# Kernel tuning notes

Measured on AMD Instinct MI355X. Metric: run time of the kernel, lower is better.

## Reference

```python
import jax, jax.numpy as jnp
import numpy as np

N, Z, CC = 32, 128, 16
NODE_SIZES = [128, 512, 2048, 8192, 32768, 67615]  # coarse -> fine
IN_CHS = [144, 80, 48, 32, 24]   # FGL input channels (after content concat)
OUT_CHS = [64, 32, 16, 8, 1]     # FGL output channels
N_S, N_T, N_C = 20, 50, 200
EPS = 1e-5


def setup_inputs() -> dict:
    key = jax.random.key(0)
    ks = jax.random.split(key, 64)
    d = {}
    d['z'] = jax.random.normal(ks[0], (N, Z), jnp.float32)
    d['svec'] = jax.random.randint(ks[1], (N,), 0, N_S)
    d['tvec'] = jax.random.randint(ks[2], (N,), 0, N_T)
    d['cvec'] = jax.random.randint(ks[3], (N,), 0, N_C)
    d['study_emb'] = 0.1 * jax.random.normal(ks[4], (N_S, CC), jnp.float32)
    d['task_emb'] = 0.1 * jax.random.normal(ks[5], (N_T, CC), jnp.float32)
    d['contrast_emb'] = 0.1 * jax.random.normal(ks[6], (N_C, CC), jnp.float32)
    fc_ins = [CC, 2 * CC, 3 * CC, 3 * CC, 3 * CC]
    for i, fi in enumerate(fc_ins):
        d[f'fc{i}_w'] = jax.random.normal(ks[7 + i], (fi, CC), jnp.float32) / np.sqrt(fi)
        d[f'fc{i}_b'] = jnp.zeros((CC,), jnp.float32)
    for i in range(5):
        d[f'w{i}'] = jax.random.normal(ks[12 + i], (OUT_CHS[i], IN_CHS[i]), jnp.float32) / np.sqrt(IN_CHS[i])
        d[f'bb{i}'] = jnp.zeros((OUT_CHS[i],), jnp.float32)
    for i in range(4):
        d[f'g{i}'] = jnp.ones((OUT_CHS[i],), jnp.float32)
        d[f'be{i}'] = jnp.zeros((OUT_CHS[i],), jnp.float32)
    # tree upsampling: each fine node has exactly one coarse parent
    for i in range(5):
        d[f'p{i}'] = jax.random.randint(ks[20 + i], (NODE_SIZES[i + 1],), 0, NODE_SIZES[i])
    return d


def _forward(z, svec, tvec, cvec, study_emb, task_emb, contrast_emb,
             fc0_w, fc0_b, fc1_w, fc1_b, fc2_w, fc2_b, fc3_w, fc3_b, fc4_w, fc4_b,
             w0, bb0, w1, bb1, w2, bb2, w3, bb3, w4, bb4,
             g0, be0, g1, be1, g2, be2, g3, be3,
             p0, p1, p2, p3, p4):
    se = study_emb[svec]
    te = task_emb[tvec]
    ce = contrast_emb[cvec]
    cat2 = jnp.concatenate([se, te], axis=1)
    cat3 = jnp.concatenate([se, te, ce], axis=1)
    contents = [se @ fc0_w + fc0_b,
                cat2 @ fc1_w + fc1_b,
                cat3 @ fc2_w + fc2_b,
                cat3 @ fc3_w + fc3_b,
                cat3 @ fc4_w + fc4_b]  # each (N, CC); dropout is identity at eval
    n = z.shape[0]
    cur = jnp.broadcast_to(z[:, :, None], (n, Z, NODE_SIZES[0]))  # (N, 128, 128)
    Ws = [w0, w1, w2, w3, w4]
    bs = [bb0, bb1, bb2, bb3, bb4]
    parents = [p0, p1, p2, p3, p4]
    bns = [(g0, be0), (g1, be1), (g2, be2), (g3, be3)]
    for i in range(5):
        c = jnp.broadcast_to(contents[i][:, :, None], (n, CC, cur.shape[2]))
        x = jnp.concatenate([cur, c], axis=1)  # (N, IN_CHS[i], nodes_in)
        # shared per-layer channel mix; mix first (cheaper), then gather by parent
        h = jnp.einsum('ncj,oc->noj', x, Ws[i]) + bs[i][None, :, None]
        cur = h[:, :, parents[i]]  # (N, OUT_CHS[i], nodes_out)
        if i < 4:
            cur = jnp.where(cur >= 0, cur, 0.2 * cur)  # LeakyReLU(0.2)
            g, be = bns[i]
            mean = cur.mean(axis=(0, 2), keepdims=True)
            var = cur.var(axis=(0, 2), keepdims=True)
            cur = g[None, :, None] * (cur - mean) * jax.lax.rsqrt(var + EPS) + be[None, :, None]
        else:
            cur = jnp.tanh(cur)
    return cur[:, 0, :]  # (N, masked_nnz)


def reference(z, svec, tvec, cvec, study_emb, task_emb, contrast_emb,
              fc0_w, fc0_b, fc1_w, fc1_b, fc2_w, fc2_b, fc3_w, fc3_b, fc4_w, fc4_b,
              w0, bb0, w1, bb1, w2, bb2, w3, bb3, w4, bb4,
              g0, be0, g1, be1, g2, be2, g3, be3,
              p0, p1, p2, p3, p4):
    return _forward(z, svec, tvec, cvec, study_emb, task_emb, contrast_emb,
                    fc0_w, fc0_b, fc1_w, fc1_b, fc2_w, fc2_b, fc3_w, fc3_b, fc4_w, fc4_b,
                    w0, bb0, w1, bb1, w2, bb2, w3, bb3, w4, bb4,
                    g0, be0, g1, be1, g2, be2, g3, be3,
                    p0, p1, p2, p3, p4)
```

## Files before the change

### kernel.cpp

```cpp
#include <hip/hip_runtime.h>
#include <hip/hip_bf16.h>

typedef __hip_bfloat16 bf16;
#define NT 512
#define ROW 67615


__device__ __forceinline__ float lo16(unsigned int u) {
  return __builtin_bit_cast(float, u << 16);
}
__device__ __forceinline__ float hi16(unsigned int u) {
  return __builtin_bit_cast(float, u & 0xFFFF0000u);
}
__device__ __forceinline__ float bs2f(unsigned short u) {
  return __builtin_bit_cast(float, ((unsigned int)u) << 16);
}
__device__ __forceinline__ unsigned short f2bs(float f) {
  return __builtin_bit_cast(unsigned short, __float2bfloat16(f));
}
__device__ __forceinline__ float gld(const void* p, int i, int isbf) {
  if (isbf) return bs2f(((const unsigned short*)p)[i]);
  return ((const float*)p)[i];
}

__device__ __forceinline__ void stage_us(unsigned short* dst, const void* src,
                                         int len, int isbf, int tid) {
  if (isbf) {
    const unsigned short* s = (const unsigned short*)src;
    for (int i = tid; i < len; i += NT) dst[i] = s[i];
  } else {
    const float* s = (const float*)src;
    for (int i = tid; i < len; i += NT) dst[i] = f2bs(s[i]);
  }
}

__device__ __forceinline__ void stageW_rt(unsigned short* dst, const void* src,
                                          int OUT, int COLS, int isbf, int tid) {
  int oshift = 31 - __clz(OUT);
  int tasks = OUT * (COLS >> 2);
  for (int j = tid; j < tasks; j += NT) {
    int o = j & (OUT - 1), c4 = j >> oshift;
    ushort4 q;
    if (isbf) {
      q = *(const ushort4*)((const unsigned short*)src + o * COLS + 4 * c4);
    } else {
      float4 v = *(const float4*)((const float*)src + o * COLS + 4 * c4);
      q = make_ushort4(f2bs(v.x), f2bs(v.y), f2bs(v.z), f2bs(v.w));
    }
    *(ushort4*)(dst + (c4 * OUT + o) * 4) = q;
  }
}

struct Params {
  const void* z;
  const int *sv, *tv, *cv;
  const void *se, *te, *ce;
  const void *fcw[5], *fcb[5];
  const void *w[5],  *wb[5];
  const void *g[4],  *be[4];
  float* t;
};

__device__ __noinline__ void do_level(
    int tid, int isbf, int INC, int OUT, int FCIN, int IS,
    const float* __restrict__ curin, float* __restrict__ curout,
    float* __restrict__ cont, const float* __restrict__ cat,
    float* __restrict__ A, float* __restrict__ Bv,
    unsigned short* __restrict__ wl,
    const void* fcw, const void* fcb, const void* W, const void* Wb,
    const void* g, const void* be, float* __restrict__ tout)
{
  const int OFF_FCB = FCIN * 16;
  const int OFF_W   = OFF_FCB + 16;
  const int OFF_WB  = OFF_W + (INC + 16) * OUT;

  stage_us(wl, fcw, FCIN * 16, isbf, tid);
  stage_us(wl + OFF_FCB, fcb, 16, isbf, tid);
  if (OUT == 1) {
    stage_us(wl + OFF_W, W, INC + 16, isbf, tid);
    stage_us(wl + OFF_WB, Wb, 1, isbf, tid);
  } else {
    stageW_rt(wl + OFF_W, W, OUT, INC + 16, isbf, tid);
    stage_us(wl + OFF_WB, Wb, OUT, isbf, tid);
    stage_us(wl + OFF_WB + OUT, g, OUT, isbf, tid);
    stage_us(wl + OFF_WB + 2 * OUT, be, OUT, isbf, tid);
  }
  __syncthreads();

  if (tid < 128) {
    int n = tid >> 2, cg = tid & 3;
    float a0 = bs2f(wl[OFF_FCB + 4 * cg]);
    float a1 = bs2f(wl[OFF_FCB + 4 * cg + 1]);
    float a2 = bs2f(wl[OFF_FCB + 4 * cg + 2]);
    float a3 = bs2f(wl[OFF_FCB + 4 * cg + 3]);
    const float4* catp = (const float4*)(cat + n * 52);
    int nk4 = FCIN >> 2;
#pragma unroll 4
    for (int k4 = 0; k4 < nk4; k4++) {
      float4 cv = catp[k4];
      float xs[4] = {cv.x, cv.y, cv.z, cv.w};
#pragma unroll
      for (int j = 0; j < 4; j++) {
        uint2 u = *(const uint2*)(wl + (4 * k4 + j) * 16 + 4 * cg);
        a0 += xs[j] * lo16(u.x); a1 += xs[j] * hi16(u.x);
        a2 += xs[j] * lo16(u.y); a3 += xs[j] * hi16(u.y);
      }
    }
    *(float4*)(cont + n * 20 + 4 * cg) = make_float4(a0, a1, a2, a3);
  }
  __syncthreads();

  if (OUT == 1) {
    if (tid < 32) {
      int n = tid;
      float s = bs2f(wl[OFF_WB]);
#pragma unroll
      for (int c = 0; c < 8; c++) s += curin[n * 68 + c] * bs2f(wl[OFF_W + c]);
#pragma unroll
      for (int k = 0; k < 16; k++) s += cont[n * 20 + k] * bs2f(wl[OFF_W + 8 + k]);
      tout[n] = tanhf(s);
    }
    return;
  }

  int TO = OUT >> 1;
  int toshift = 31 - __clz(TO);
  const uint4* Wp = (const uint4*)(wl + OFF_W);
  if (tid < 16 * TO) {
    int tn = tid >> toshift, to = tid & (TO - 1);
    int n0 = 2 * tn, o0 = 2 * to;
    const float4* X0 = (const float4*)(curin + n0 * IS);
    const float4* X1 = (const float4*)(curin + (n0 + 1) * IS);
    const float4* C0 = (const float4*)(cont + n0 * 20);
    const float4* C1 = (const float4*)(cont + (n0 + 1) * 20);
    float b0 = bs2f(wl[OFF_WB + o0]), b1 = bs2f(wl[OFF_WB + o0 + 1]);
    float s00 = b0, s01 = b1, s10 = b0, s11 = b1;
    int nc4 = INC >> 2;
#pragma unroll 4
    for (int c4 = 0; c4 < nc4; c4++) {
      float4 xa = X0[c4], xb = X1[c4];
      uint4 u = Wp[c4 * TO + to];
      float wa0 = lo16(u.x), wa1 = hi16(u.x), wa2 = lo16(u.y), wa3 = hi16(u.y);
      float wb0 = lo16(u.z), wb1 = hi16(u.z), wb2 = lo16(u.w), wb3 = hi16(u.w);
      s00 += xa.x * wa0 + xa.y * wa1 + xa.z * wa2 + xa.w * wa3;
      s01 += xa.x * wb0 + xa.y * wb1 + xa.z * wb2 + xa.w * wb3;
      s10 += xb.x * wa0 + xb.y * wa1 + xb.z * wa2 + xb.w * wa3;
      s11 += xb.x * wb0 + xb.y * wb1 + xb.z * wb2 + xb.w * wb3;
    }
#pragma unroll 4
    for (int k4 = 0; k4 < 4; k4++) {
      float4 xa = C0[k4], xb = C1[k4];
      uint4 u = Wp[(nc4 + k4) * TO + to];
      float wa0 = lo16(u.x), wa1 = hi16(u.x), wa2 = lo16(u.y), wa3 = hi16(u.y);
      float wb0 = lo16(u.z), wb1 = hi16(u.z), wb2 = lo16(u.w), wb3 = hi16(u.w);
      s00 += xa.x * wa0 + xa.y * wa1 + xa.z * wa2 + xa.w * wa3;
      s01 += xa.x * wb0 + xa.y * wb1 + xa.z * wb2 + xa.w * wb3;
      s10 += xb.x * wa0 + xb.y * wa1 + xb.z * wa2 + xb.w * wa3;
      s11 += xb.x * wb0 + xb.y * wb1 + xb.z * wb2 + xb.w * wb3;
    }
    s00 = s00 >= 0.f ? s00 : 0.2f * s00;
    s01 = s01 >= 0.f ? s01 : 0.2f * s01;
    s10 = s10 >= 0.f ? s10 : 0.2f * s10;
    s11 = s11 >= 0.f ? s11 : 0.2f * s11;
    curout[n0 * 68 + o0]           = s00;
    curout[n0 * 68 + o0 + 1]       = s01;
    curout[(n0 + 1) * 68 + o0]     = s10;
    curout[(n0 + 1) * 68 + o0 + 1] = s11;
  }
  __syncthreads();

  if (tid < OUT) {
    int o = tid;
    float su = 0.f, sq = 0.f;
#pragma unroll 4
    for (int n = 0; n < 32; n++) { float v = curout[n * 68 + o]; su += v; sq += v * v; }
    float mean = su * (1.f / 32.f);
    float var  = fmaxf(sq * (1.f / 32.f) - mean * mean, 0.f);
    float inv  = rsqrtf(var + 1e-5f);
    float a = bs2f(wl[OFF_WB + OUT + o]) * inv;
    A[o]  = a;
    Bv[o] = bs2f(wl[OFF_WB + 2 * OUT + o]) - mean * a;
  }
  __syncthreads();
  for (int i = tid; i < 32 * OUT; i += NT) {
    int n = i >> (toshift + 1), o = i & (OUT - 1);
    curout[n * 68 + o] = A[o] * curout[n * 68 + o] + Bv[o];
  }
  __syncthreads();
}

__global__ __launch_bounds__(NT) void head_kernel(Params P) {
  __shared__ __align__(16) float zl[32 * 128];
  __shared__ __align__(16) float cat[32 * 52];
  __shared__ __align__(16) float cont[32 * 20];
  __shared__ __align__(16) float act0[32 * 68];
  __shared__ __align__(16) float act1[32 * 68];
  __shared__ float A[64], Bv[64];
  __shared__ __align__(16) unsigned short wl[9680];
  __shared__ int sOK;
  int tid = threadIdx.x;

  if (tid == 0) sOK = 1;
  __syncthreads();
  if (tid < 64) {
    unsigned int w = ((const unsigned int*)P.z)[tid];
    float a = fabsf(bs2f((unsigned short)(w & 0xFFFFu)));
    if (!(a == 0.0f || (a >= 1e-12f && a <= 1e4f))) atomicAnd(&sOK, 0);
  }
  __syncthreads();
  const int isbf = sOK;
  if (tid == 0) ((int*)P.t)[32] = isbf;

  if (isbf) {
    const uint4* s = (const uint4*)P.z;
    for (int j = tid; j < 512; j += NT) {
      uint4 u = s[j];
      *(float4*)(zl + 8 * j)     = make_float4(lo16(u.x), hi16(u.x), lo16(u.y), hi16(u.y));
      *(float4*)(zl + 8 * j + 4) = make_float4(lo16(u.z), hi16(u.z), lo16(u.w), hi16(u.w));
    }
  } else {
    const float4* s = (const float4*)P.z;
    for (int j = tid; j < 1024; j += NT) *(float4*)(zl + 4 * j) = s[j];
  }
  if (tid < 512) {
    int n = tid >> 4, c = tid & 15;
    cat[n * 52 + c]      = gld(P.se, P.sv[n] * 16 + c, isbf);
    cat[n * 52 + 16 + c] = gld(P.te, P.tv[n] * 16 + c, isbf);
    cat[n * 52 + 32 + c] = gld(P.ce, P.cv[n] * 16 + c, isbf);
  }

  do_level(tid, isbf, 128, 64, 16, 128, zl,   act0, cont, cat, A, Bv, wl,
           P.fcw[0], P.fcb[0], P.w[0], P.wb[0], P.g[0], P.be[0], P.t);
  do_level(tid, isbf,  64, 32, 32,  68, act0, act1, cont, cat, A, Bv, wl,
           P.fcw[1], P.fcb[1], P.w[1], P.wb[1], P.g[1], P.be[1], P.t);
  do_level(tid, isbf,  32, 16, 48,  68, act1, act0, cont, cat, A, Bv, wl,
           P.fcw[2], P.fcb[2], P.w[2], P.wb[2], P.g[2], P.be[2], P.t);
  do_level(tid, isbf,  16,  8, 48,  68, act0, act1, cont, cat, A, Bv, wl,
           P.fcw[3], P.fcb[3], P.w[3], P.wb[3], P.g[3], P.be[3], P.t);
  do_level(tid, isbf,   8,  1, 48,  68, act1, act0, cont, cat, A, Bv, wl,
           P.fcw[4], P.fcb[4], P.w[4], P.wb[4], P.g[0], P.be[0], P.t);
}

__global__ __launch_bounds__(256) void bcast_kernel(const float* __restrict__ t,
                                                    void* __restrict__ outv) {
  int n = blockIdx.y;
  int isbf = ((const int*)t)[32];
  float tv = t[n];
  int chunk = blockIdx.x * 256 + threadIdx.x;

  if (isbf) {
    unsigned short us = f2bs(tv);
    unsigned int u2 = ((unsigned int)us << 16) | (unsigned int)us;
    uint4 v4 = make_uint4(u2, u2, u2, u2);
    unsigned short* row = (unsigned short*)outv + (size_t)n * ROW;
    int s = (int)((16u - ((unsigned int)(unsigned long long)row & 15u)) & 15u) >> 1;
    int e = s + chunk * 8;
    if (e + 8 <= ROW) *(uint4*)(row + e) = v4;
    if (blockIdx.x == 0 && threadIdx.x == 0) {
      for (int i = 0; i < s; i++) row[i] = us;
      int nch = (ROW - s) >> 3;
      for (int i = s + nch * 8; i < ROW; i++) row[i] = us;
    }
  } else {
    float* row = (float*)outv + (size_t)n * ROW;
    int s = (int)((16u - ((unsigned int)(unsigned long long)row & 15u)) & 15u) >> 2;
    int e = s + chunk * 4;
    if (e + 4 <= ROW) *(float4*)(row + e) = make_float4(tv, tv, tv, tv);
    if (blockIdx.x == 0 && threadIdx.x == 0) {
      for (int i = 0; i < s; i++) row[i] = tv;
      int nch = (ROW - s) >> 2;
      for (int i = s + nch * 4; i < ROW; i++) row[i] = tv;
    }
  }
}

extern "C" void kernel_launch(void* const* d_in, const int* in_sizes, int n_in,
                              void* d_out, int out_size, void* d_ws, size_t ws_size,
                              hipStream_t stream) {
  Params P;
  P.z  = d_in[0];
  P.sv = (const int*)d_in[1];
  P.tv = (const int*)d_in[2];
  P.cv = (const int*)d_in[3];
  P.se = d_in[4];
  P.te = d_in[5];
  P.ce = d_in[6];
  for (int i = 0; i < 5; i++) {
    P.fcw[i] = d_in[7 + 2 * i];
    P.fcb[i] = d_in[8 + 2 * i];
  }
  for (int i = 0; i < 5; i++) {
    P.w[i]  = d_in[17 + 2 * i];
    P.wb[i] = d_in[18 + 2 * i];
  }
  for (int i = 0; i < 4; i++) {
    P.g[i]  = d_in[27 + 2 * i];
    P.be[i] = d_in[28 + 2 * i];
  }
  P.t = (float*)d_ws;

  hipLaunchKernelGGL(head_kernel, dim3(1), dim3(NT), 0, stream, P);
  hipLaunchKernelGGL(bcast_kernel, dim3(67, 32), dim3(256), 0, stream,
                     (const float*)d_ws, d_out);
}
```

Baseline: 168.3 us.

## Fuse head MLP and broadcast into one kernel with redundant per-block head

Merges the single-block head kernel and the broadcast kernel into one launch. Each of the 8x32 blocks recomputes the small MLP/BN chain redundantly, then writes its chunk of one output row. All levels' weights are staged into shared memory in one pass, and all five content FCs are computed together. Levels are templated for compile-time sizes and full unrolling. This removes a kernel launch and the workspace round trip, at the cost of repeating the head work in every block and using more dynamic shared memory.

```diff
diff --git a/kernel.cpp b/kernel.cpp
--- a/kernel.cpp
+++ b/kernel.cpp
@@ -58,86 +58,37 @@
   const void *fcw[5], *fcb[5];
   const void *w[5],  *wb[5];
   const void *g[4],  *be[4];
-  float* t;
+  void* out;
 };
 
-__device__ __noinline__ void do_level(
-    int tid, int isbf, int INC, int OUT, int FCIN, int IS,
+#define WLB0 0
+#define WLB1 9680
+#define WLB2 12864
+#define WLB3 14464
+#define WLB4 15528
+#define WL_TOT 16344
+
+template<int INC, int OUT, int IS>
+__device__ __forceinline__ void level_bn(int tid,
     const float* __restrict__ curin, float* __restrict__ curout,
-    float* __restrict__ cont, const float* __restrict__ cat,
-    float* __restrict__ A, float* __restrict__ Bv,
-    unsigned short* __restrict__ wl,
-    const void* fcw, const void* fcb, const void* W, const void* Wb,
-    const void* g, const void* be, float* __restrict__ tout)
+    const float* __restrict__ contl, const unsigned short* __restrict__ wlv,
+    float* __restrict__ A, float* __restrict__ Bv)
 {
-  const int OFF_FCB = FCIN * 16;
-  const int OFF_W   = OFF_FCB + 16;
-  const int OFF_WB  = OFF_W + (INC + 16) * OUT;
-
-  stage_us(wl, fcw, FCIN * 16, isbf, tid);
-  stage_us(wl + OFF_FCB, fcb, 16, isbf, tid);
-  if (OUT == 1) {
-    stage_us(wl + OFF_W, W, INC + 16, isbf, tid);
-    stage_us(wl + OFF_WB, Wb, 1, isbf, tid);
-  } else {
-    stageW_rt(wl + OFF_W, W, OUT, INC + 16, isbf, tid);
-    stage_us(wl + OFF_WB, Wb, OUT, isbf, tid);
-    stage_us(wl + OFF_WB + OUT, g, OUT, isbf, tid);
-    stage_us(wl + OFF_WB + 2 * OUT, be, OUT, isbf, tid);
-  }
-  __syncthreads();
-
-  if (tid < 128) {
-    int n = tid >> 2, cg = tid & 3;
-    float a0 = bs2f(wl[OFF_FCB + 4 * cg]);
-    float a1 = bs2f(wl[OFF_FCB + 4 * cg + 1]);
-    float a2 = bs2f(wl[OFF_FCB + 4 * cg + 2]);
-    float a3 = bs2f(wl[OFF_FCB + 4 * cg + 3]);
-    const float4* catp = (const float4*)(cat + n * 52);
-    int nk4 = FCIN >> 2;
-#pragma unroll 4
-    for (int k4 = 0; k4 < nk4; k4++) {
-      float4 cv = catp[k4];
-      float xs[4] = {cv.x, cv.y, cv.z, cv.w};
-#pragma unroll
-      for (int j = 0; j < 4; j++) {
-        uint2 u = *(const uint2*)(wl + (4 * k4 + j) * 16 + 4 * cg);
-        a0 += xs[j] * lo16(u.x); a1 += xs[j] * hi16(u.x);
-        a2 += xs[j] * lo16(u.y); a3 += xs[j] * hi16(u.y);
-      }
-    }
-    *(float4*)(cont + n * 20 + 4 * cg) = make_float4(a0, a1, a2, a3);
-  }
-  __syncthreads();
-
-  if (OUT == 1) {
-    if (tid < 32) {
-      int n = tid;
-      float s = bs2f(wl[OFF_WB]);
-#pragma unroll
-      for (int c = 0; c < 8; c++) s += curin[n * 68 + c] * bs2f(wl[OFF_W + c]);
-#pragma unroll
-      for (int k = 0; k < 16; k++) s += cont[n * 20 + k] * bs2f(wl[OFF_W + 8 + k]);
-      tout[n] = tanhf(s);
-    }
-    return;
-  }
-
-  int TO = OUT >> 1;
-  int toshift = 31 - __clz(TO);
-  const uint4* Wp = (const uint4*)(wl + OFF_W);
+  constexpr int COLS = INC + 16;
+  constexpr int OFF_WB = COLS * OUT;
+  constexpr int TO = OUT / 2;
+  const uint4* Wp = (const uint4*)wlv;
   if (tid < 16 * TO) {
-    int tn = tid >> toshift, to = tid & (TO - 1);
+    int tn = tid / TO, to = tid % TO;
     int n0 = 2 * tn, o0 = 2 * to;
     const float4* X0 = (const float4*)(curin + n0 * IS);
     const float4* X1 = (const float4*)(curin + (n0 + 1) * IS);
-    const float4* C0 = (const float4*)(cont + n0 * 20);
-    const float4* C1 = (const float4*)(cont + (n0 + 1) * 20);
-    float b0 = bs2f(wl[OFF_WB + o0]), b1 = bs2f(wl[OFF_WB + o0 + 1]);
+    const float4* C0 = (const float4*)(contl + n0 * 20);
+    const float4* C1 = (const float4*)(contl + (n0 + 1) * 20);
+    float b0 = bs2f(wlv[OFF_WB + o0]), b1 = bs2f(wlv[OFF_WB + o0 + 1]);
     float s00 = b0, s01 = b1, s10 = b0, s11 = b1;
-    int nc4 = INC >> 2;
-#pragma unroll 4
-    for (int c4 = 0; c4 < nc4; c4++) {
+#pragma unroll
+    for (int c4 = 0; c4 < INC / 4; c4++) {
       float4 xa = X0[c4], xb = X1[c4];
       uint4 u = Wp[c4 * TO + to];
       float wa0 = lo16(u.x), wa1 = hi16(u.x), wa2 = lo16(u.y), wa3 = hi16(u.y);
@@ -147,10 +98,10 @@
       s10 += xb.x * wa0 + xb.y * wa1 + xb.z * wa2 + xb.w * wa3;
       s11 += xb.x * wb0 + xb.y * wb1 + xb.z * wb2 + xb.w * wb3;
     }
-#pragma unroll 4
+#pragma unroll
     for (int k4 = 0; k4 < 4; k4++) {
       float4 xa = C0[k4], xb = C1[k4];
-      uint4 u = Wp[(nc4 + k4) * TO + to];
+      uint4 u = Wp[(INC / 4 + k4) * TO + to];
       float wa0 = lo16(u.x), wa1 = hi16(u.x), wa2 = lo16(u.y), wa3 = hi16(u.y);
       float wb0 = lo16(u.z), wb1 = hi16(u.z), wb2 = lo16(u.w), wb3 = hi16(u.w);
       s00 += xa.x * wa0 + xa.y * wa1 + xa.z * wa2 + xa.w * wa3;
@@ -168,35 +119,37 @@
     curout[(n0 + 1) * 68 + o0 + 1] = s11;
   }
   __syncthreads();
-
   if (tid < OUT) {
     int o = tid;
     float su = 0.f, sq = 0.f;
-#pragma unroll 4
+#pragma unroll 8
     for (int n = 0; n < 32; n++) { float v = curout[n * 68 + o]; su += v; sq += v * v; }
     float mean = su * (1.f / 32.f);
     float var  = fmaxf(sq * (1.f / 32.f) - mean * mean, 0.f);
     float inv  = rsqrtf(var + 1e-5f);
-    float a = bs2f(wl[OFF_WB + OUT + o]) * inv;
+    float a = bs2f(wlv[OFF_WB + OUT + o]) * inv;
     A[o]  = a;
-    Bv[o] = bs2f(wl[OFF_WB + 2 * OUT + o]) - mean * a;
+    Bv[o] = bs2f(wlv[OFF_WB + 2 * OUT + o]) - mean * a;
   }
   __syncthreads();
   for (int i = tid; i < 32 * OUT; i += NT) {
-    int n = i >> (toshift + 1), o = i & (OUT - 1);
+    int n = i / OUT, o = i % OUT;
     curout[n * 68 + o] = A[o] * curout[n * 68 + o] + Bv[o];
   }
   __syncthreads();
 }
 
-__global__ __launch_bounds__(NT) void head_kernel(Params P) {
-  __shared__ __align__(16) float zl[32 * 128];
-  __shared__ __align__(16) float cat[32 * 52];
-  __shared__ __align__(16) float cont[32 * 20];
-  __shared__ __align__(16) float act0[32 * 68];
-  __shared__ __align__(16) float act1[32 * 68];
-  __shared__ float A[64], Bv[64];
-  __shared__ __align__(16) unsigned short wl[9680];
+__global__ __launch_bounds__(NT) void fused_kernel(Params P) {
+  extern __shared__ __align__(16) char smem[];
+  float* zl   = (float*)smem;
+  float* cat  = zl + 4096;
+  float* cont = cat + 1664;
+  float* act0 = cont + 3200;
+  float* act1 = act0 + 2176;
+  float* A    = act1 + 2176;
+  float* Bv   = A + 64;
+  float* tsh  = Bv + 64;
+  unsigned short* wl = (unsigned short*)(tsh + 32);
   __shared__ int sOK;
   int tid = threadIdx.x;
 
@@ -209,67 +162,134 @@
   }
   __syncthreads();
   const int isbf = sOK;
-  if (tid == 0) ((int*)P.t)[32] = isbf;
 
   if (isbf) {
     const uint4* s = (const uint4*)P.z;
-    for (int j = tid; j < 512; j += NT) {
-      uint4 u = s[j];
-      *(float4*)(zl + 8 * j)     = make_float4(lo16(u.x), hi16(u.x), lo16(u.y), hi16(u.y));
-      *(float4*)(zl + 8 * j + 4) = make_float4(lo16(u.z), hi16(u.z), lo16(u.w), hi16(u.w));
+    if (tid < 512) {
+      uint4 u = s[tid];
+      *(float4*)(zl + 8 * tid)     = make_float4(lo16(u.x), hi16(u.x), lo16(u.y), hi16(u.y));
+      *(float4*)(zl + 8 * tid + 4) = make_float4(lo16(u.z), hi16(u.z), lo16(u.w), hi16(u.w));
     }
   } else {
     const float4* s = (const float4*)P.z;
     for (int j = tid; j < 1024; j += NT) *(float4*)(zl + 4 * j) = s[j];
   }
-  if (tid < 512) {
+  {
     int n = tid >> 4, c = tid & 15;
     cat[n * 52 + c]      = gld(P.se, P.sv[n] * 16 + c, isbf);
     cat[n * 52 + 16 + c] = gld(P.te, P.tv[n] * 16 + c, isbf);
     cat[n * 52 + 32 + c] = gld(P.ce, P.cv[n] * 16 + c, isbf);
   }
-
-  do_level(tid, isbf, 128, 64, 16, 128, zl,   act0, cont, cat, A, Bv, wl,
-           P.fcw[0], P.fcb[0], P.w[0], P.wb[0], P.g[0], P.be[0], P.t);
-  do_level(tid, isbf,  64, 32, 32,  68, act0, act1, cont, cat, A, Bv, wl,
-           P.fcw[1], P.fcb[1], P.w[1], P.wb[1], P.g[1], P.be[1], P.t);
-  do_level(tid, isbf,  32, 16, 48,  68, act1, act0, cont, cat, A, Bv, wl,
-           P.fcw[2], P.fcb[2], P.w[2], P.wb[2], P.g[2], P.be[2], P.t);
-  do_level(tid, isbf,  16,  8, 48,  68, act0, act1, cont, cat, A, Bv, wl,
-           P.fcw[3], P.fcb[3], P.w[3], P.wb[3], P.g[3], P.be[3], P.t);
-  do_level(tid, isbf,   8,  1, 48,  68, act1, act0, cont, cat, A, Bv, wl,
-           P.fcw[4], P.fcb[4], P.w[4], P.wb[4], P.g[0], P.be[0], P.t);
-}
-
-__global__ __launch_bounds__(256) void bcast_kernel(const float* __restrict__ t,
-                                                    void* __restrict__ outv) {
-  int n = blockIdx.y;
-  int isbf = ((const int*)t)[32];
-  float tv = t[n];
-  int chunk = blockIdx.x * 256 + threadIdx.x;
+  stage_us(wl + WLB0,            P.fcw[0], 256, isbf, tid);
+  stage_us(wl + WLB0 + 256,      P.fcb[0], 16,  isbf, tid);
+  stageW_rt(wl + WLB0 + 272,     P.w[0], 64, 144, isbf, tid);
+  stage_us(wl + WLB0 + 272 + 9216, P.wb[0], 64, isbf, tid);
+  stage_us(wl + WLB0 + 272 + 9280, P.g[0],  64, isbf, tid);
+  stage_us(wl + WLB0 + 272 + 9344, P.be[0], 64, isbf, tid);
+  stage_us(wl + WLB1,            P.fcw[1], 512, isbf, tid);
+  stage_us(wl + WLB1 + 512,      P.fcb[1], 16,  isbf, tid);
+  stageW_rt(wl + WLB1 + 528,     P.w[1], 32, 80, isbf, tid);
+  stage_us(wl + WLB1 + 528 + 2560, P.wb[1], 32, isbf, tid);
+  stage_us(wl + WLB1 + 528 + 2592, P.g[1],  32, isbf, tid);
+  stage_us(wl + WLB1 + 528 + 2624, P.be[1], 32, isbf, tid);
+  stage_us(wl + WLB2,            P.fcw[2], 768, isbf, tid);
+  stage_us(wl + WLB2 + 768,      P.fcb[2], 16,  isbf, tid);
+  stageW_rt(wl + WLB2 + 784,     P.w[2], 16, 48, isbf, tid);
+  stage_us(wl + WLB2 + 784 + 768, P.wb[2], 16, isbf, tid);
+  stage_us(wl + WLB2 + 784 + 784, P.g[2],  16, isbf, tid);
+  stage_us(wl + WLB2 + 784 + 800, P.be[2], 16, isbf, tid);
+  stage_us(wl + WLB3,            P.fcw[3], 768, isbf, tid);
+  stage_us(wl + WLB3 + 768,      P.fcb[3], 16,  isbf, tid);
+  stageW_rt(wl + WLB3 + 784,     P.w[3], 8, 32, isbf, tid);
+  stage_us(wl + WLB3 + 784 + 256, P.wb[3], 8, isbf, tid);
+  stage_us(wl + WLB3 + 784 + 264, P.g[3],  8, isbf, tid);
+  stage_us(wl + WLB3 + 784 + 272, P.be[3], 8, isbf, tid);
+  stage_us(wl + WLB4,            P.fcw[4], 768, isbf, tid);
+  stage_us(wl + WLB4 + 768,      P.fcb[4], 16,  isbf, tid);
+  stage_us(wl + WLB4 + 784,      P.w[4],   24,  isbf, tid);
+  stage_us(wl + WLB4 + 808,      P.wb[4],  1,   isbf, tid);
+  __syncthreads();
+
+  for (int i = tid; i < 640; i += NT) {
+    int lvl = i >> 7, r = i & 127, n = r >> 2, cg = r & 3;
+    int fcin = (lvl >= 2) ? 48 : (16 << lvl);
+    int wb = (lvl == 0) ? WLB0 : (lvl == 1) ? WLB1 : (lvl == 2) ? WLB2
+           : (lvl == 3) ? WLB3 : WLB4;
+    const unsigned short* fw = wl + wb;
+    int offfcb = fcin * 16;
+    float a0 = bs2f(fw[offfcb + 4 * cg]);
+    float a1 = bs2f(fw[offfcb + 4 * cg + 1]);
+    float a2 = bs2f(fw[offfcb + 4 * cg + 2]);
+    float a3 = bs2f(fw[offfcb + 4 * cg + 3]);
+    const float4* catp = (const float4*)(cat + n * 52);
+    int nk4 = fcin >> 2;
+#pragma unroll 4
+    for (int k4 = 0; k4 < nk4; k4++) {
+      float4 cv = catp[k4];
+      float xs[4] = {cv.x, cv.y, cv.z, cv.w};
+#pragma unroll
+      for (int j = 0; j < 4; j++) {
+        uint2 u = *(const uint2*)(fw + (4 * k4 + j) * 16 + 4 * cg);
+        a0 += xs[j] * lo16(u.x); a1 += xs[j] * hi16(u.x);
+        a2 += xs[j] * lo16(u.y); a3 += xs[j] * hi16(u.y);
+      }
+    }
+    *(float4*)(cont + lvl * 640 + n * 20 + 4 * cg) = make_float4(a0, a1, a2, a3);
+  }
+  __syncthreads();
+
+  level_bn<128, 64, 128>(tid, zl,   act0, cont,        wl + WLB0 + 272, A, Bv);
+  level_bn< 64, 32,  68>(tid, act0, act1, cont + 640,  wl + WLB1 + 528, A, Bv);
+  level_bn< 32, 16,  68>(tid, act1, act0, cont + 1280, wl + WLB2 + 784, A, Bv);
+  level_bn< 16,  8,  68>(tid, act0, act1, cont + 1920, wl + WLB3 + 784, A, Bv);
+  if (tid < 32) {
+    const unsigned short* w4 = wl + WLB4 + 784;
+    float s = bs2f(wl[WLB4 + 808]);
+#pragma unroll
+    for (int c = 0; c < 8; c++) s += act1[tid * 68 + c] * bs2f(w4[c]);
+#pragma unroll
+    for (int k = 0; k < 16; k++) s += cont[2560 + tid * 20 + k] * bs2f(w4[8 + k]);
+    tsh[tid] = tanhf(s);
+  }
+  __syncthreads();
+
+  int row = blockIdx.y;
+  float tv = tsh[row];
+  const int CHUNK = 8452;
+  int c0 = blockIdx.x * CHUNK;
+  int c1 = c0 + CHUNK; if (c1 > ROW) c1 = ROW;
 
   if (isbf) {
     unsigned short us = f2bs(tv);
     unsigned int u2 = ((unsigned int)us << 16) | (unsigned int)us;
     uint4 v4 = make_uint4(u2, u2, u2, u2);
-    unsigned short* row = (unsigned short*)outv + (size_t)n * ROW;
-    int s = (int)((16u - ((unsigned int)(unsigned long long)row & 15u)) & 15u) >> 1;
-    int e = s + chunk * 8;
-    if (e + 8 <= ROW) *(uint4*)(row + e) = v4;
-    if (blockIdx.x == 0 && threadIdx.x == 0) {
-      for (int i = 0; i < s; i++) row[i] = us;
-      int nch = (ROW - s) >> 3;
-      for (int i = s + nch * 8; i < ROW; i++) row[i] = us;
+    unsigned short* rowp = (unsigned short*)P.out + (size_t)row * ROW;
+    unsigned long long addr = (unsigned long long)(rowp + c0);
+    int s = (int)((16u - ((unsigned int)addr & 15u)) & 15u) >> 1;
+    int vstart = c0 + s;
+    for (int e = vstart + tid * 8; e + 8 <= c1; e += NT * 8) *(uint4*)(rowp + e) = v4;
+    if (tid == 0) {
+      int hend = vstart < c1 ? vstart : c1;
+      for (int i = c0; i < hend; i++) rowp[i] = us;
+      if (c1 > vstart) {
+        int ts = vstart + (((c1 - vstart) >> 3) << 3);
+        for (int i = ts; i < c1; i++) rowp[i] = us;
+      }
     }
   } else {
-    float* row = (float*)outv + (size_t)n * ROW;
-    int s = (int)((16u - ((unsigned int)(unsigned long long)row & 15u)) & 15u) >> 2;
-    int e = s + chunk * 4;
-    if (e + 4 <= ROW) *(float4*)(row + e) = make_float4(tv, tv, tv, tv);
-    if (blockIdx.x == 0 && threadIdx.x == 0) {
-      for (int i = 0; i < s; i++) row[i] = tv;
-      int nch = (ROW - s) >> 2;
-      for (int i = s + nch * 4; i < ROW; i++) row[i] = tv;
+    float* rowp = (float*)P.out + (size_t)row * ROW;
+    unsigned long long addr = (unsigned long long)(rowp + c0);
+    int s = (int)((16u - ((unsigned int)addr & 15u)) & 15u) >> 2;
+    int vstart = c0 + s;
+    float4 v4 = make_float4(tv, tv, tv, tv);
+    for (int e = vstart + tid * 4; e + 4 <= c1; e += NT * 4) *(float4*)(rowp + e) = v4;
+    if (tid == 0) {
+      int hend = vstart < c1 ? vstart : c1;
+      for (int i = c0; i < hend; i++) rowp[i] = tv;
+      if (c1 > vstart) {
+        int ts = vstart + (((c1 - vstart) >> 2) << 2);
+        for (int i = ts; i < c1; i++) rowp[i] = tv;
+      }
     }
   }
 }
@@ -297,9 +317,8 @@
     P.g[i]  = d_in[27 + 2 * i];
     P.be[i] = d_in[28 + 2 * i];
   }
-  P.t = (float*)d_ws;
-
-  hipLaunchKernelGGL(head_kernel, dim3(1), dim3(NT), 0, stream, P);
-  hipLaunchKernelGGL(bcast_kernel, dim3(67, 32), dim3(256), 0, stream,
-                     (const float*)d_ws, d_out);
-}
+  P.out = d_out;
+
+  size_t smem = 13472 * 4 + WL_TOT * 2;
+  hipLaunchKernelGGL(fused_kernel, dim3(8, 32), dim3(NT), smem, stream, P);
+}
```

Result: faster. 161.1 us (-4.3%).
